# Kernel tuning notes

Measured on AMD Instinct MI355X. Metric: run time of the kernel, lower is better.

The kernel has to match this reference:

```python
import jax, jax.numpy as jnp
import numpy as np
from jax import lax

N = 8192      # nodes == batch (forward cats node and batch embeddings)
E = 262144    # edges, avg degree 32
T = 32        # seq_len
DD = 16       # dynamic_feature_dim
DS = 128      # static_feature_dim
GH = 64       # gnn_hidden_dim
RH = 128      # rnn_hidden_dim
L = 10        # output_lead_times
EPS = 1e-5


def setup_inputs() -> dict:
    key = jax.random.key(0)
    ks = jax.random.split(key, 32)
    def rn(i, shape, s=0.05):
        return jax.random.normal(ks[i], shape, jnp.float32) * s
    return {
        "dynamic_features": rn(0, (N, T, DD), 1.0),
        "x_static": rn(1, (N, DS), 1.0),
        "edge_index": jax.random.randint(ks[2], (2, E), 0, N, jnp.int32),
        "gcn1_w": rn(3, (DS, GH)), "gcn1_b": rn(4, (GH,)),
        "gcn2_w": rn(5, (GH, GH)), "gcn2_b": rn(6, (GH,)),
        "bn1_g": 1.0 + rn(7, (GH,)), "bn1_b": rn(8, (GH,)),
        "bn2_g": 1.0 + rn(9, (GH,)), "bn2_b": rn(10, (GH,)),
        "w_ih0": rn(11, (4 * RH, DD)), "w_hh0": rn(12, (4 * RH, RH)),
        "b_ih0": rn(13, (4 * RH,)), "b_hh0": rn(14, (4 * RH,)),
        "w_ih1": rn(15, (4 * RH, RH)), "w_hh1": rn(16, (4 * RH, RH)),
        "b_ih1": rn(17, (4 * RH,)), "b_hh1": rn(18, (4 * RH,)),
        "fc1_w": rn(19, (GH + RH, 128)), "fc1_b": rn(20, (128,)),
        "fbn_g": 1.0 + rn(21, (128,)), "fbn_b": rn(22, (128,)),
        "fc2_w": rn(23, (128, 64)), "fc2_b": rn(24, (64,)),
        "out_w": rn(25, (64, L)), "out_b": rn(26, (L,)),
    }


def _gcn(x, w, b, src, dst, n):
    h = x @ w
    loops = jnp.arange(n, dtype=src.dtype)
    s = jnp.concatenate([src, loops])
    d = jnp.concatenate([dst, loops])
    deg = jax.ops.segment_sum(jnp.ones(s.shape[0], x.dtype), d, num_segments=n)
    dis = lax.rsqrt(jnp.maximum(deg, 1.0))
    msg = h[s] * (dis[s] * dis[d])[:, None]
    return jax.ops.segment_sum(msg, d, num_segments=n) + b


def _bn(x, g, b):
    # eval-mode BatchNorm1d: running_mean=0, running_var=1
    return x * (g * lax.rsqrt(jnp.asarray(1.0 + EPS, x.dtype))) + b


def _lstm_layer(xp, w_hh):
    # xp: [B, T, 4H] input projection with both biases already added
    B = xp.shape[0]
    H = w_hh.shape[1]
    h0 = jnp.zeros((B, H), xp.dtype)
    c0 = jnp.zeros((B, H), xp.dtype)
    def step(carry, xt):
        h, c = carry
        gates = xt + h @ w_hh.T  # torch gate order: i, f, g, o
        i, f, g, o = jnp.split(gates, 4, axis=-1)
        c = jax.nn.sigmoid(f) * c + jax.nn.sigmoid(i) * jnp.tanh(g)
        h = jax.nn.sigmoid(o) * jnp.tanh(c)
        return (h, c), h
    _, hs = lax.scan(step, (h0, c0), jnp.swapaxes(xp, 0, 1))
    return jnp.swapaxes(hs, 0, 1)  # [B, T, H]


def _forward(dynamic_features, x_static, edge_index,
             gcn1_w, gcn1_b, gcn2_w, gcn2_b, bn1_g, bn1_b, bn2_g, bn2_b,
             w_ih0, w_hh0, b_ih0, b_hh0, w_ih1, w_hh1, b_ih1, b_hh1,
             fc1_w, fc1_b, fbn_g, fbn_b, fc2_w, fc2_b, out_w, out_b):
    src, dst = edge_index[0], edge_index[1]
    n = x_static.shape[0]
    # GNN branch (dropout = eval-mode identity)
    h = _gcn(x_static, gcn1_w, gcn1_b, src, dst, n)
    h = jax.nn.relu(_bn(h, bn1_g, bn1_b))
    h = _gcn(h, gcn2_w, gcn2_b, src, dst, n)
    gnn_emb = jax.nn.relu(_bn(h, bn2_g, bn2_b))
    # 2-layer LSTM branch
    xp0 = jnp.einsum('btd,gd->btg', dynamic_features, w_ih0) + b_ih0 + b_hh0
    h1 = _lstm_layer(xp0, w_hh0)
    xp1 = jnp.einsum('bth,gh->btg', h1, w_ih1) + b_ih1 + b_hh1
    h2 = _lstm_layer(xp1, w_hh1)
    rnn_emb = h2[:, -1, :]
    # fusion MLP
    fused = jnp.concatenate([gnn_emb, rnn_emb], axis=1)
    x = jax.nn.relu(_bn(fused @ fc1_w + fc1_b, fbn_g, fbn_b))
    x = jax.nn.relu(x @ fc2_w + fc2_b)
    return x @ out_w + out_b


def reference(dynamic_features, x_static, edge_index,
              gcn1_w, gcn1_b, gcn2_w, gcn2_b, bn1_g, bn1_b, bn2_g, bn2_b,
              w_ih0, w_hh0, b_ih0, b_hh0, w_ih1, w_hh1, b_ih1, b_hh1,
              fc1_w, fc1_b, fbn_g, fbn_b, fc2_w, fc2_b, out_w, out_b):
    return _forward(dynamic_features, x_static, edge_index,
                    gcn1_w, gcn1_b, gcn2_w, gcn2_b, bn1_g, bn1_b, bn2_g, bn2_b,
                    w_ih0, w_hh0, b_ih0, b_hh0, w_ih1, w_hh1, b_ih1, b_hh1,
                    fc1_w, fc1_b, fbn_g, fbn_b, fc2_w, fc2_b, out_w, out_b)
```

## Files before the change

### kernel.cpp

```cpp
#include <hip/hip_runtime.h>
#include <hip/hip_bf16.h>

#define NN 8192
#define NE 262144

typedef float v2 __attribute__((ext_vector_type(2)));
typedef float v4 __attribute__((ext_vector_type(4)));
typedef float f4 __attribute__((ext_vector_type(4)));
typedef _Float16 h8 __attribute__((ext_vector_type(8)));
typedef _Float16 h4 __attribute__((ext_vector_type(4)));

__device__ __forceinline__ float rcp_(float x) { return __builtin_amdgcn_rcpf(x); }
__device__ __forceinline__ float ew(float iv, float fv, float gv, float ov, float& c) {
    float F = __expf(-fv);
    float I = __expf(-iv);
    float G = __expf(2.0f * gv);
    c = c * rcp_(1.0f + F) + (G - 1.0f) * rcp_((G + 1.0f) * (1.0f + I));
    float O = __expf(-ov);
    float E = __expf(2.0f * c);
    return (E - 1.0f) * rcp_((E + 1.0f) * (1.0f + O));
}

__global__ void k_prep_all(const float* __restrict__ dyn,
                           const float* __restrict__ wih0, const float* __restrict__ whh0,
                           const float* __restrict__ bih0, const float* __restrict__ bhh0,
                           const float* __restrict__ wih1, const float* __restrict__ whh1,
                           const float* __restrict__ bih1, const float* __restrict__ bhh1,
                           const int* __restrict__ dst,
                           _Float16* __restrict__ dyn16, _Float16* __restrict__ WB0h,
                           _Float16* __restrict__ TLg, _Float16* __restrict__ WB1,
                           float* __restrict__ bias, int* __restrict__ cnt) {
    int b = blockIdx.x, tid = threadIdx.x;
    if (b < 4096) {
        int i = b * 256 + tid;
        f4 v = *(const f4*)(dyn + (size_t)i * 4);
        h4 o = {(_Float16)v[0], (_Float16)v[1], (_Float16)v[2], (_Float16)v[3]};
        *(h4*)(dyn16 + (size_t)i * 4) = o;
    } else if (b < 4900) {
        int i = (b - 4096) * 256 + tid;
        if (i < 65536) {
            int idx = i & 7, col = (i >> 3) & 511, kgq = (i >> 12) & 3, kt = i >> 14;
            int kh = kt * 32 + kgq * 8 + idx;
            WB0h[i] = (_Float16)whh0[col * 128 + kh];
        } else if (i < 73728) {
            int m = i - 65536;
            int kd = m & 15, g = m >> 4;
            TLg[m] = (_Float16)wih0[g * 16 + kd];
        } else if (i < 204800) {
            int m = i - 73728;
            int kt = m >> 14, rem = m & 16383, g = rem >> 5, kk = rem & 31, k = kt * 32 + kk;
            WB1[m] = (_Float16)((k < 128) ? wih1[g * 128 + k] : whh1[g * 128 + (k - 128)]);
        } else {
            int g = i - 204800;
            bias[g] = (g < 512) ? (bih0[g] + bhh0[g]) : (bih1[g - 512] + bhh1[g - 512]);
        }
    } else {
        int e = (b - 4900) * 256 + tid;
        if (e < NE) atomicAdd(&cnt[dst[e]], 1);
    }
}

__global__ __launch_bounds__(1024) void k_scan(const int* __restrict__ cnt, int* __restrict__ rowstart,
                                               float* __restrict__ dis) {
    __shared__ int part[1024];
    int t = threadIdx.x;
    int base = t * 8, s = 0, loc[8];
#pragma unroll
    for (int i = 0; i < 8; ++i) { loc[i] = s; s += cnt[base + i]; }
    part[t] = s;
    __syncthreads();
    for (int off = 1; off < 1024; off <<= 1) {
        int v = part[t];
        int add = (t >= off) ? part[t - off] : 0;
        __syncthreads();
        part[t] = v + add;
        __syncthreads();
    }
    int pre = (t == 0) ? 0 : part[t - 1];
#pragma unroll
    for (int i = 0; i < 8; ++i) {
        rowstart[base + i] = pre + loc[i];
        dis[base + i] = rsqrtf((float)(cnt[base + i] + 1));
    }
    if (t == 1023) rowstart[8192] = NE;
}
__global__ void k_fill(const int* __restrict__ src, const int* __restrict__ dst,
                       const int* __restrict__ rowstart, int* __restrict__ cursor,
                       int* __restrict__ srcidx) {
    int e = blockIdx.x * 256 + threadIdx.x;
    if (e < NE) {
        int d = dst[e];
        int pos = rowstart[d] + atomicAdd(&cursor[d], 1);
        srcidx[pos] = src[e];
    }
}
__global__ __launch_bounds__(256) void k_gcn_gemm(const float* __restrict__ in, const float* __restrict__ w,
                                                  const float* __restrict__ dis, float* __restrict__ hs, int K) {
    int wv = threadIdx.x >> 6, ln = threadIdx.x & 63;
    int row = blockIdx.x * 4 + wv;
    const float* xp = in + (size_t)row * K;
    float a = 0.f;
#pragma unroll 4
    for (int k = 0; k < K; ++k) a += xp[k] * w[k * 64 + ln];
    hs[(size_t)row * 64 + ln] = a * dis[row];
}
__global__ __launch_bounds__(256) void k_gather_gemm(const float* __restrict__ hs, const int* __restrict__ srcidx,
                                                     const int* __restrict__ rowstart, const float* __restrict__ dis,
                                                     const float* __restrict__ gb, const float* __restrict__ bng,
                                                     const float* __restrict__ bnb, const float* __restrict__ g2w,
                                                     float* __restrict__ hs2) {
    int ln = threadIdx.x & 63;
    int d = (blockIdx.x * 256 + threadIdx.x) >> 6;
    float acc = hs[(size_t)d * 64 + ln];
    int b = rowstart[d], e = rowstart[d + 1];
    int i = b;
    for (; i + 4 <= e; i += 4) {
        int s0 = srcidx[i], s1 = srcidx[i + 1], s2 = srcidx[i + 2], s3 = srcidx[i + 3];
        acc += hs[(size_t)s0 * 64 + ln];
        acc += hs[(size_t)s1 * 64 + ln];
        acc += hs[(size_t)s2 * 64 + ln];
        acc += hs[(size_t)s3 * 64 + ln];
    }
    for (; i < e; ++i) acc += hs[(size_t)srcidx[i] * 64 + ln];
    float rs = rsqrtf(1.0f + 1e-5f);
    float y = acc * dis[d] + gb[ln];
    y = fmaxf(y * (bng[ln] * rs) + bnb[ln], 0.f);
    float a2 = 0.f;
#pragma unroll 8
    for (int k = 0; k < 64; ++k) a2 += __shfl(y, k, 64) * g2w[k * 64 + ln];
    hs2[(size_t)d * 64 + ln] = a2 * dis[d];
}
__global__ __launch_bounds__(256) void k_gather(const float* __restrict__ hs, const int* __restrict__ srcidx,
                                                const int* __restrict__ rowstart, const float* __restrict__ dis,
                                                const float* __restrict__ gb, const float* __restrict__ bng,
                                                const float* __restrict__ bnb, float* __restrict__ out) {
    int ln = threadIdx.x & 63;
    int d = (blockIdx.x * 256 + threadIdx.x) >> 6;
    float acc = hs[(size_t)d * 64 + ln];
    int b = rowstart[d], e = rowstart[d + 1];
    int i = b;
    for (; i + 4 <= e; i += 4) {
        int s0 = srcidx[i], s1 = srcidx[i + 1], s2 = srcidx[i + 2], s3 = srcidx[i + 3];
        acc += hs[(size_t)s0 * 64 + ln];
        acc += hs[(size_t)s1 * 64 + ln];
        acc += hs[(size_t)s2 * 64 + ln];
        acc += hs[(size_t)s3 * 64 + ln];
    }
    for (; i < e; ++i) acc += hs[(size_t)srcidx[i] * 64 + ln];
    float rs = rsqrtf(1.0f + 1e-5f);
    float v = acc * dis[d] + gb[ln];
    v = v * (bng[ln] * rs) + bnb[ln];
    out[(size_t)d * 64 + ln] = fmaxf(v, 0.f);
}

__device__ __forceinline__ h8 ldx(const _Float16* xs, int buf, int row, int chunk) {
    return *(const h8*)((const char*)xs + buf * 16384 + row * 512 + ((chunk ^ (row & 7)) << 4));
}
__device__ __forceinline__ void wrx(_Float16* xs, int buf, int row, int col, _Float16 v) {
    *(_Float16*)((char*)xs + buf * 16384 + row * 512 + ((((col >> 3) ^ (row & 7))) << 4) + (col & 7) * 2) = v;
}

__global__ __launch_bounds__(512, 2) void k_lstm(const _Float16* __restrict__ dyn16,
                                                 const _Float16* __restrict__ WB0h,
                                                 const _Float16* __restrict__ TLg,
                                                 const _Float16* __restrict__ WB1,
                                                 const float* __restrict__ bias,
                                                 float* __restrict__ rnn) {
    __shared__ __align__(16) _Float16 wb0[65536];
    __shared__ __align__(16) _Float16 xs[16384];

    const int tid = threadIdx.x;
    const int wv = tid >> 6, ln = tid & 63;
    const int lr = ln & 15, kg = ln >> 4;
    const int j = wv * 16 + lr;
    const int row0 = blockIdx.x * 32;

    for (int i = tid; i < 8192; i += 512) ((v4*)wb0)[i] = ((const v4*)WB0h)[i];
    for (int i = tid; i < 16384; i += 512) xs[i] = (_Float16)0.f;

    h8 b1r[8][4];
#pragma unroll
    for (int kt = 0; kt < 8; ++kt)
#pragma unroll
        for (int q = 0; q < 4; ++q)
            b1r[kt][q] = *(const h8*)(WB1 + (size_t)kt * 16384 + (q * 128 + j) * 32 + kg * 8);
    h8 bt[4];
#pragma unroll
    for (int q = 0; q < 4; ++q)
        bt[q] = *(const h8*)(TLg + (q * 128 + j) * 16 + (kg & 1) * 8);

    float b0q[4], b1q[4];
#pragma unroll
    for (int q = 0; q < 4; ++q) { b0q[q] = bias[q * 128 + j]; b1q[q] = bias[512 + q * 128 + j]; }
    float c0[2][4], c1[2][4];
#pragma unroll
    for (int mt = 0; mt < 2; ++mt)
#pragma unroll
        for (int r = 0; r < 4; ++r) { c0[mt][r] = 0.f; c1[mt][r] = 0.f; }

    h8 dreg[2];
#pragma unroll
    for (int mt = 0; mt < 2; ++mt)
#pragma unroll
        for (int e = 0; e < 8; ++e) dreg[mt][e] = (_Float16)0.f;
    if (kg < 2) {
#pragma unroll
        for (int mt = 0; mt < 2; ++mt)
            dreg[mt] = *(const h8*)(dyn16 + (size_t)(row0 + mt * 16 + lr) * 512 + (kg & 1) * 8);
    }
    __syncthreads();

    {
        f4 acc[2][4];
#pragma unroll
        for (int q = 0; q < 4; ++q) { f4 z = {b0q[q], b0q[q], b0q[q], b0q[q]}; acc[0][q] = z; acc[1][q] = z; }
#pragma unroll
        for (int q = 0; q < 4; ++q) {
            acc[0][q] = __builtin_amdgcn_mfma_f32_16x16x32_f16(dreg[0], bt[q], acc[0][q], 0, 0, 0);
            acc[1][q] = __builtin_amdgcn_mfma_f32_16x16x32_f16(dreg[1], bt[q], acc[1][q], 0, 0, 0);
        }
#pragma unroll
        for (int mt = 0; mt < 2; ++mt)
#pragma unroll
            for (int r = 0; r < 4; ++r) {
                float h = ew(acc[mt][0][r], acc[mt][1][r], acc[mt][2][r], acc[mt][3][r], c0[mt][r]);
                wrx(xs, 0, mt * 16 + kg * 4 + r, j, (_Float16)h);
            }
        if (kg < 2) {
#pragma unroll
            for (int mt = 0; mt < 2; ++mt)
                dreg[mt] = *(const h8*)(dyn16 + (size_t)(row0 + mt * 16 + lr) * 512 + 16 + (kg & 1) * 8);
        }
    }

#pragma unroll 1
    for (int i = 0; i < 31; ++i) {
        const int cur = i & 1, old = cur ^ 1;
        __syncthreads();
        f4 acc[2][4];
#pragma unroll
        for (int q = 0; q < 4; ++q) { f4 z = {b1q[q], b1q[q], b1q[q], b1q[q]}; acc[0][q] = z; acc[1][q] = z; }
#pragma unroll
        for (int kt = 0; kt < 8; ++kt) {
            const int bufA = (kt < 4) ? cur : old;
            const int ch = (kt < 4) ? (kt * 4 + kg) : (16 + (kt - 4) * 4 + kg);
            h8 a0 = ldx(xs, bufA, lr, ch);
            h8 a1 = ldx(xs, bufA, 16 + lr, ch);
#pragma unroll
            for (int q = 0; q < 4; ++q) {
                acc[0][q] = __builtin_amdgcn_mfma_f32_16x16x32_f16(a0, b1r[kt][q], acc[0][q], 0, 0, 0);
                acc[1][q] = __builtin_amdgcn_mfma_f32_16x16x32_f16(a1, b1r[kt][q], acc[1][q], 0, 0, 0);
            }
        }
#pragma unroll
        for (int mt = 0; mt < 2; ++mt)
#pragma unroll
            for (int r = 0; r < 4; ++r) {
                float h = ew(acc[mt][0][r], acc[mt][1][r], acc[mt][2][r], acc[mt][3][r], c1[mt][r]);
                wrx(xs, cur, mt * 16 + kg * 4 + r, 128 + j, (_Float16)h);
            }
#pragma unroll
        for (int q = 0; q < 4; ++q) { f4 z = {b0q[q], b0q[q], b0q[q], b0q[q]}; acc[0][q] = z; acc[1][q] = z; }
#pragma unroll
        for (int kt = 0; kt < 4; ++kt) {
            h8 a0 = ldx(xs, cur, lr, kt * 4 + kg);
            h8 a1 = ldx(xs, cur, 16 + lr, kt * 4 + kg);
            h8 bq[4];
#pragma unroll
            for (int q = 0; q < 4; ++q)
                bq[q] = *(const h8*)(wb0 + (size_t)(((kt * 4 + kg) * 512 + q * 128 + j) * 8));
#pragma unroll
            for (int q = 0; q < 4; ++q) {
                acc[0][q] = __builtin_amdgcn_mfma_f32_16x16x32_f16(a0, bq[q], acc[0][q], 0, 0, 0);
                acc[1][q] = __builtin_amdgcn_mfma_f32_16x16x32_f16(a1, bq[q], acc[1][q], 0, 0, 0);
            }
        }
#pragma unroll
        for (int q = 0; q < 4; ++q) {
            acc[0][q] = __builtin_amdgcn_mfma_f32_16x16x32_f16(dreg[0], bt[q], acc[0][q], 0, 0, 0);
            acc[1][q] = __builtin_amdgcn_mfma_f32_16x16x32_f16(dreg[1], bt[q], acc[1][q], 0, 0, 0);
        }
#pragma unroll
        for (int mt = 0; mt < 2; ++mt)
#pragma unroll
            for (int r = 0; r < 4; ++r) {
                float h = ew(acc[mt][0][r], acc[mt][1][r], acc[mt][2][r], acc[mt][3][r], c0[mt][r]);
                wrx(xs, old, mt * 16 + kg * 4 + r, j, (_Float16)h);
            }
        if (i < 30 && kg < 2) {
#pragma unroll
            for (int mt = 0; mt < 2; ++mt)
                dreg[mt] = *(const h8*)(dyn16 + (size_t)(row0 + mt * 16 + lr) * 512 + (i + 2) * 16 + (kg & 1) * 8);
        }
    }
    __syncthreads();
    {
        const int cur = 1, old = 0;
        f4 acc[2][4];
#pragma unroll
        for (int q = 0; q < 4; ++q) { f4 z = {b1q[q], b1q[q], b1q[q], b1q[q]}; acc[0][q] = z; acc[1][q] = z; }
#pragma unroll
        for (int kt = 0; kt < 8; ++kt) {
            const int bufA = (kt < 4) ? cur : old;
            const int ch = (kt < 4) ? (kt * 4 + kg) : (16 + (kt - 4) * 4 + kg);
            h8 a0 = ldx(xs, bufA, lr, ch);
            h8 a1 = ldx(xs, bufA, 16 + lr, ch);
#pragma unroll
            for (int q = 0; q < 4; ++q) {
                acc[0][q] = __builtin_amdgcn_mfma_f32_16x16x32_f16(a0, b1r[kt][q], acc[0][q], 0, 0, 0);
                acc[1][q] = __builtin_amdgcn_mfma_f32_16x16x32_f16(a1, b1r[kt][q], acc[1][q], 0, 0, 0);
            }
        }
#pragma unroll
        for (int mt = 0; mt < 2; ++mt)
#pragma unroll
            for (int r = 0; r < 4; ++r) {
                float h = ew(acc[mt][0][r], acc[mt][1][r], acc[mt][2][r], acc[mt][3][r], c1[mt][r]);
                rnn[(size_t)(row0 + mt * 16 + kg * 4 + r) * 128 + j] = h;
            }
    }
}

__global__ __launch_bounds__(256) void k_head(const float* __restrict__ gnn, const float* __restrict__ rnn,
                                              const float* __restrict__ fc1w, const float* __restrict__ fc1b,
                                              const float* __restrict__ fbng, const float* __restrict__ fbnb,
                                              const float* __restrict__ fc2w, const float* __restrict__ fc2b,
                                              const float* __restrict__ outw, const float* __restrict__ outb,
                                              float* __restrict__ out) {
    __shared__ __align__(16) float xin[32][196];
    __shared__ __align__(16) float xh2[32][132];
    __shared__ __align__(16) float xh3[32][68];
    const int tid = threadIdx.x;
    const int r0 = blockIdx.x * 32;
    for (int i = tid; i < 32 * 64; i += 256) { int r = i >> 6, c = i & 63; xin[r][c] = gnn[(size_t)(r0 + r) * 64 + c]; }
    for (int i = tid; i < 32 * 128; i += 256) { int r = i >> 7, c = i & 127; xin[r][64 + c] = rnn[(size_t)(r0 + r) * 128 + c]; }
    __syncthreads();
    const int wv = tid >> 6, ln = tid & 63, wr = wv * 8;
    const float rs = rsqrtf(1.0f + 1e-5f);
    float a[8][2];
    float b0 = fc1b[2 * ln], b1 = fc1b[2 * ln + 1];
#pragma unroll
    for (int r = 0; r < 8; ++r) { a[r][0] = b0; a[r][1] = b1; }
    for (int k = 0; k < 192; ++k) {
        v2 w = *(const v2*)&fc1w[k * 128 + 2 * ln];
#pragma unroll
        for (int r = 0; r < 8; ++r) { float x = xin[wr + r][k]; a[r][0] += x * w[0]; a[r][1] += x * w[1]; }
    }
    float s0 = fbng[2 * ln] * rs, s1 = fbng[2 * ln + 1] * rs;
    float bb0 = fbnb[2 * ln], bb1 = fbnb[2 * ln + 1];
#pragma unroll
    for (int r = 0; r < 8; ++r) {
        v2 h;
        h[0] = fmaxf(a[r][0] * s0 + bb0, 0.f);
        h[1] = fmaxf(a[r][1] * s1 + bb1, 0.f);
        *(v2*)&xh2[wr + r][2 * ln] = h;
    }
    __syncthreads();
    float a2[8];
    float b2 = fc2b[ln];
#pragma unroll
    for (int r = 0; r < 8; ++r) a2[r] = b2;
    for (int k = 0; k < 128; ++k) {
        float w = fc2w[k * 64 + ln];
#pragma unroll
        for (int r = 0; r < 8; ++r) a2[r] += xh2[wr + r][k] * w;
    }
#pragma unroll
    for (int r = 0; r < 8; ++r) xh3[wr + r][ln] = fmaxf(a2[r], 0.f);
    __syncthreads();
    if (ln < 10) {
#pragma unroll
        for (int r = 0; r < 8; ++r) {
            float a3 = outb[ln];
            for (int k = 0; k < 64; ++k) a3 += xh3[wr + r][k] * outw[k * 10 + ln];
            out[(size_t)(r0 + wr + r) * 10 + ln] = a3;
        }
    }
}

extern "C" void kernel_launch(void* const* d_in, const int* in_sizes, int n_in,
                              void* d_out, int out_size, void* d_ws, size_t ws_size,
                              hipStream_t stream) {
    const float* dyn  = (const float*)d_in[0];
    const float* xs_  = (const float*)d_in[1];
    const int*   ei   = (const int*)d_in[2];
    const float* g1w  = (const float*)d_in[3];
    const float* g1b  = (const float*)d_in[4];
    const float* g2w  = (const float*)d_in[5];
    const float* g2b  = (const float*)d_in[6];
    const float* bn1g = (const float*)d_in[7];
    const float* bn1b = (const float*)d_in[8];
    const float* bn2g = (const float*)d_in[9];
    const float* bn2b = (const float*)d_in[10];
    const float* wih0 = (const float*)d_in[11];
    const float* whh0 = (const float*)d_in[12];
    const float* bih0 = (const float*)d_in[13];
    const float* bhh0 = (const float*)d_in[14];
    const float* wih1 = (const float*)d_in[15];
    const float* whh1 = (const float*)d_in[16];
    const float* bih1 = (const float*)d_in[17];
    const float* bhh1 = (const float*)d_in[18];
    const float* fc1w = (const float*)d_in[19];
    const float* fc1b = (const float*)d_in[20];
    const float* fbng = (const float*)d_in[21];
    const float* fbnb = (const float*)d_in[22];
    const float* fc2w = (const float*)d_in[23];
    const float* fc2b = (const float*)d_in[24];
    const float* outw = (const float*)d_in[25];
    const float* outb = (const float*)d_in[26];
    float* out = (float*)d_out;

    char* ws = (char*)d_ws;
    _Float16* WB0h  = (_Float16*)(ws + 0);
    _Float16* TLg   = (_Float16*)(ws + 131072);
    _Float16* WB1   = (_Float16*)(ws + 147456);
    _Float16* dyn16 = (_Float16*)(ws + 409600);
    float* fbase = (float*)(ws + 8798208);
    float* bias = fbase;
    float* dis  = fbase + 1024;
    float* hs   = fbase + 9216;
    float* hs2  = fbase + 533504;
    float* gnn  = fbase + 1057792;
    float* rnn  = fbase + 1582080;
    int* ibase   = (int*)(ws + 19320832);
    int* cnt     = ibase;
    int* cursor  = ibase + 8192;
    int* rowstart= ibase + 16384;
    int* srcidx  = ibase + 24592;

    const int* srcp = ei;
    const int* dstp = ei + NE;

    hipMemsetAsync(cnt, 0, 2 * 8192 * sizeof(int), stream);
    k_prep_all<<<5924, 256, 0, stream>>>(dyn, wih0, whh0, bih0, bhh0, wih1, whh1, bih1, bhh1,
                                         dstp, dyn16, WB0h, TLg, WB1, bias, cnt);
    k_scan<<<1, 1024, 0, stream>>>(cnt, rowstart, dis);
    k_fill<<<1024, 256, 0, stream>>>(srcp, dstp, rowstart, cursor, srcidx);
    k_gcn_gemm<<<2048, 256, 0, stream>>>(xs_, g1w, dis, hs, 128);
    k_gather_gemm<<<2048, 256, 0, stream>>>(hs, srcidx, rowstart, dis, g1b, bn1g, bn1b, g2w, hs2);
    k_gather<<<2048, 256, 0, stream>>>(hs2, srcidx, rowstart, dis, g2b, bn2g, bn2b, gnn);
    k_lstm<<<256, 512, 0, stream>>>(dyn16, WB0h, TLg, WB1, bias, rnn);
    k_head<<<256, 256, 0, stream>>>(gnn, rnn, fc1w, fc1b, fbng, fbnb, fc2w, fc2b, outw, outb, out);
}
```

Baseline: 297.4 us.

## Fold first GCN GEMM into prep kernel, rework LSTM activations and prefetch

The first GCN projection now runs inside the prep kernel as extra blocks, without degree scaling. This removes one kernel launch and lets the GEMM overlap with the edge counting. Because of that, the gather kernels now multiply each neighbour row by dis[s], which adds a per-edge load. The LSTM cell math is rewritten with separate sigmoid and tanh helpers, and the dynamic-feature prefetch for step i+2 is moved to the start of the loop body to hide its latency. The new activations use more exp and reciprocal calls than the old fused formula.

Result: slower. 311.2 us (+4.6%).

```diff
diff --git a/kernel.cpp b/kernel.cpp
--- a/kernel.cpp
+++ b/kernel.cpp
@@ -11,15 +11,8 @@
 typedef _Float16 h4 __attribute__((ext_vector_type(4)));
 
 __device__ __forceinline__ float rcp_(float x) { return __builtin_amdgcn_rcpf(x); }
-__device__ __forceinline__ float ew(float iv, float fv, float gv, float ov, float& c) {
-    float F = __expf(-fv);
-    float I = __expf(-iv);
-    float G = __expf(2.0f * gv);
-    c = c * rcp_(1.0f + F) + (G - 1.0f) * rcp_((G + 1.0f) * (1.0f + I));
-    float O = __expf(-ov);
-    float E = __expf(2.0f * c);
-    return (E - 1.0f) * rcp_((E + 1.0f) * (1.0f + O));
-}
+__device__ __forceinline__ float sigm(float x) { return rcp_(1.0f + __expf(-x)); }
+__device__ __forceinline__ float tanh_(float x) { return 1.0f - 2.0f * rcp_(__expf(2.0f * x) + 1.0f); }
 
 __global__ void k_prep_all(const float* __restrict__ dyn,
                            const float* __restrict__ wih0, const float* __restrict__ whh0,
@@ -27,9 +20,11 @@
                            const float* __restrict__ wih1, const float* __restrict__ whh1,
                            const float* __restrict__ bih1, const float* __restrict__ bhh1,
                            const int* __restrict__ dst,
+                           const float* __restrict__ xs_, const float* __restrict__ g1w,
                            _Float16* __restrict__ dyn16, _Float16* __restrict__ WB0h,
                            _Float16* __restrict__ TLg, _Float16* __restrict__ WB1,
-                           float* __restrict__ bias, int* __restrict__ cnt) {
+                           float* __restrict__ bias, int* __restrict__ cnt,
+                           float* __restrict__ hs_raw) {
     int b = blockIdx.x, tid = threadIdx.x;
     if (b < 4096) {
         int i = b * 256 + tid;
@@ -54,9 +49,17 @@
             int g = i - 204800;
             bias[g] = (g < 512) ? (bih0[g] + bhh0[g]) : (bih1[g - 512] + bhh1[g - 512]);
         }
-    } else {
+    } else if (b < 5924) {
         int e = (b - 4900) * 256 + tid;
         if (e < NE) atomicAdd(&cnt[dst[e]], 1);
+    } else {
+        int wv = tid >> 6, ln = tid & 63;
+        int row = (b - 5924) * 4 + wv;
+        const float* xp = xs_ + (size_t)row * 128;
+        float a = 0.f;
+#pragma unroll 4
+        for (int k = 0; k < 128; ++k) a += xp[k] * g1w[k * 64 + ln];
+        hs_raw[(size_t)row * 64 + ln] = a;
     }
 }
 
@@ -94,16 +97,6 @@
         srcidx[pos] = src[e];
     }
 }
-__global__ __launch_bounds__(256) void k_gcn_gemm(const float* __restrict__ in, const float* __restrict__ w,
-                                                  const float* __restrict__ dis, float* __restrict__ hs, int K) {
-    int wv = threadIdx.x >> 6, ln = threadIdx.x & 63;
-    int row = blockIdx.x * 4 + wv;
-    const float* xp = in + (size_t)row * K;
-    float a = 0.f;
-#pragma unroll 4
-    for (int k = 0; k < K; ++k) a += xp[k] * w[k * 64 + ln];
-    hs[(size_t)row * 64 + ln] = a * dis[row];
-}
 __global__ __launch_bounds__(256) void k_gather_gemm(const float* __restrict__ hs, const int* __restrict__ srcidx,
                                                      const int* __restrict__ rowstart, const float* __restrict__ dis,
                                                      const float* __restrict__ gb, const float* __restrict__ bng,
@@ -111,24 +104,25 @@
                                                      float* __restrict__ hs2) {
     int ln = threadIdx.x & 63;
     int d = (blockIdx.x * 256 + threadIdx.x) >> 6;
-    float acc = hs[(size_t)d * 64 + ln];
+    float dd = dis[d];
+    float acc = hs[(size_t)d * 64 + ln] * dd;
     int b = rowstart[d], e = rowstart[d + 1];
     int i = b;
     for (; i + 4 <= e; i += 4) {
         int s0 = srcidx[i], s1 = srcidx[i + 1], s2 = srcidx[i + 2], s3 = srcidx[i + 3];
-        acc += hs[(size_t)s0 * 64 + ln];
-        acc += hs[(size_t)s1 * 64 + ln];
-        acc += hs[(size_t)s2 * 64 + ln];
-        acc += hs[(size_t)s3 * 64 + ln];
-    }
-    for (; i < e; ++i) acc += hs[(size_t)srcidx[i] * 64 + ln];
+        acc += hs[(size_t)s0 * 64 + ln] * dis[s0];
+        acc += hs[(size_t)s1 * 64 + ln] * dis[s1];
+        acc += hs[(size_t)s2 * 64 + ln] * dis[s2];
+        acc += hs[(size_t)s3 * 64 + ln] * dis[s3];
+    }
+    for (; i < e; ++i) { int s = srcidx[i]; acc += hs[(size_t)s * 64 + ln] * dis[s]; }
     float rs = rsqrtf(1.0f + 1e-5f);
-    float y = acc * dis[d] + gb[ln];
+    float y = acc * dd + gb[ln];
     y = fmaxf(y * (bng[ln] * rs) + bnb[ln], 0.f);
     float a2 = 0.f;
 #pragma unroll 8
     for (int k = 0; k < 64; ++k) a2 += __shfl(y, k, 64) * g2w[k * 64 + ln];
-    hs2[(size_t)d * 64 + ln] = a2 * dis[d];
+    hs2[(size_t)d * 64 + ln] = a2;
 }
 __global__ __launch_bounds__(256) void k_gather(const float* __restrict__ hs, const int* __restrict__ srcidx,
                                                 const int* __restrict__ rowstart, const float* __restrict__ dis,
@@ -136,19 +130,20 @@
                                                 const float* __restrict__ bnb, float* __restrict__ out) {
     int ln = threadIdx.x & 63;
     int d = (blockIdx.x * 256 + threadIdx.x) >> 6;
-    float acc = hs[(size_t)d * 64 + ln];
+    float dd = dis[d];
+    float acc = hs[(size_t)d * 64 + ln] * dd;
     int b = rowstart[d], e = rowstart[d + 1];
     int i = b;
     for (; i + 4 <= e; i += 4) {
         int s0 = srcidx[i], s1 = srcidx[i + 1], s2 = srcidx[i + 2], s3 = srcidx[i + 3];
-        acc += hs[(size_t)s0 * 64 + ln];
-        acc += hs[(size_t)s1 * 64 + ln];
-        acc += hs[(size_t)s2 * 64 + ln];
-        acc += hs[(size_t)s3 * 64 + ln];
-    }
-    for (; i < e; ++i) acc += hs[(size_t)srcidx[i] * 64 + ln];
+        acc += hs[(size_t)s0 * 64 + ln] * dis[s0];
+        acc += hs[(size_t)s1 * 64 + ln] * dis[s1];
+        acc += hs[(size_t)s2 * 64 + ln] * dis[s2];
+        acc += hs[(size_t)s3 * 64 + ln] * dis[s3];
+    }
+    for (; i < e; ++i) { int s = srcidx[i]; acc += hs[(size_t)s * 64 + ln] * dis[s]; }
     float rs = rsqrtf(1.0f + 1e-5f);
-    float v = acc * dis[d] + gb[ln];
+    float v = acc * dd + gb[ln];
     v = v * (bng[ln] * rs) + bnb[ln];
     out[(size_t)d * 64 + ln] = fmaxf(v, 0.f);
 }
@@ -198,11 +193,11 @@
 #pragma unroll
         for (int r = 0; r < 4; ++r) { c0[mt][r] = 0.f; c1[mt][r] = 0.f; }
 
-    h8 dreg[2];
+    h8 dreg[2], pre[2];
 #pragma unroll
     for (int mt = 0; mt < 2; ++mt)
 #pragma unroll
-        for (int e = 0; e < 8; ++e) dreg[mt][e] = (_Float16)0.f;
+        for (int e = 0; e < 8; ++e) { dreg[mt][e] = (_Float16)0.f; pre[mt][e] = (_Float16)0.f; }
     if (kg < 2) {
 #pragma unroll
         for (int mt = 0; mt < 2; ++mt)
@@ -223,8 +218,10 @@
         for (int mt = 0; mt < 2; ++mt)
 #pragma unroll
             for (int r = 0; r < 4; ++r) {
-                float h = ew(acc[mt][0][r], acc[mt][1][r], acc[mt][2][r], acc[mt][3][r], c0[mt][r]);
-                wrx(xs, 0, mt * 16 + kg * 4 + r, j, (_Float16)h);
+                float iv = acc[mt][0][r], fv = acc[mt][1][r], gv = acc[mt][2][r], ov = acc[mt][3][r];
+                float c = sigm(fv) * c0[mt][r] + sigm(iv) * tanh_(gv);
+                c0[mt][r] = c;
+                wrx(xs, 0, mt * 16 + kg * 4 + r, j, (_Float16)(sigm(ov) * tanh_(c)));
             }
         if (kg < 2) {
 #pragma unroll
@@ -237,6 +234,11 @@
     for (int i = 0; i < 31; ++i) {
         const int cur = i & 1, old = cur ^ 1;
         __syncthreads();
+        if (i < 30 && kg < 2) {
+#pragma unroll
+            for (int mt = 0; mt < 2; ++mt)
+                pre[mt] = *(const h8*)(dyn16 + (size_t)(row0 + mt * 16 + lr) * 512 + (i + 2) * 16 + (kg & 1) * 8);
+        }
         f4 acc[2][4];
 #pragma unroll
         for (int q = 0; q < 4; ++q) { f4 z = {b1q[q], b1q[q], b1q[q], b1q[q]}; acc[0][q] = z; acc[1][q] = z; }
@@ -256,8 +258,10 @@
         for (int mt = 0; mt < 2; ++mt)
 #pragma unroll
             for (int r = 0; r < 4; ++r) {
-                float h = ew(acc[mt][0][r], acc[mt][1][r], acc[mt][2][r], acc[mt][3][r], c1[mt][r]);
-                wrx(xs, cur, mt * 16 + kg * 4 + r, 128 + j, (_Float16)h);
+                float iv = acc[mt][0][r], fv = acc[mt][1][r], gv = acc[mt][2][r], ov = acc[mt][3][r];
+                float c = sigm(fv) * c1[mt][r] + sigm(iv) * tanh_(gv);
+                c1[mt][r] = c;
+                wrx(xs, cur, mt * 16 + kg * 4 + r, 128 + j, (_Float16)(sigm(ov) * tanh_(c)));
             }
 #pragma unroll
         for (int q = 0; q < 4; ++q) { f4 z = {b0q[q], b0q[q], b0q[q], b0q[q]}; acc[0][q] = z; acc[1][q] = z; }
@@ -284,14 +288,12 @@
         for (int mt = 0; mt < 2; ++mt)
 #pragma unroll
             for (int r = 0; r < 4; ++r) {
-                float h = ew(acc[mt][0][r], acc[mt][1][r], acc[mt][2][r], acc[mt][3][r], c0[mt][r]);
-                wrx(xs, old, mt * 16 + kg * 4 + r, j, (_Float16)h);
-            }
-        if (i < 30 && kg < 2) {
-#pragma unroll
-            for (int mt = 0; mt < 2; ++mt)
-                dreg[mt] = *(const h8*)(dyn16 + (size_t)(row0 + mt * 16 + lr) * 512 + (i + 2) * 16 + (kg & 1) * 8);
-        }
+                float iv = acc[mt][0][r], fv = acc[mt][1][r], gv = acc[mt][2][r], ov = acc[mt][3][r];
+                float c = sigm(fv) * c0[mt][r] + sigm(iv) * tanh_(gv);
+                c0[mt][r] = c;
+                wrx(xs, old, mt * 16 + kg * 4 + r, j, (_Float16)(sigm(ov) * tanh_(c)));
+            }
+        if (i < 30) { dreg[0] = pre[0]; dreg[1] = pre[1]; }
     }
     __syncthreads();
     {
@@ -315,7 +317,9 @@
         for (int mt = 0; mt < 2; ++mt)
 #pragma unroll
             for (int r = 0; r < 4; ++r) {
-                float h = ew(acc[mt][0][r], acc[mt][1][r], acc[mt][2][r], acc[mt][3][r], c1[mt][r]);
+                float iv = acc[mt][0][r], fv = acc[mt][1][r], gv = acc[mt][2][r], ov = acc[mt][3][r];
+                float c = sigm(fv) * c1[mt][r] + sigm(iv) * tanh_(gv);
+                float h = sigm(ov) * tanh_(c);
                 rnn[(size_t)(row0 + mt * 16 + kg * 4 + r) * 128 + j] = h;
             }
     }
@@ -432,11 +436,10 @@
     const int* dstp = ei + NE;
 
     hipMemsetAsync(cnt, 0, 2 * 8192 * sizeof(int), stream);
-    k_prep_all<<<5924, 256, 0, stream>>>(dyn, wih0, whh0, bih0, bhh0, wih1, whh1, bih1, bhh1,
-                                         dstp, dyn16, WB0h, TLg, WB1, bias, cnt);
+    k_prep_all<<<7972, 256, 0, stream>>>(dyn, wih0, whh0, bih0, bhh0, wih1, whh1, bih1, bhh1,
+                                         dstp, xs_, g1w, dyn16, WB0h, TLg, WB1, bias, cnt, hs);
     k_scan<<<1, 1024, 0, stream>>>(cnt, rowstart, dis);
     k_fill<<<1024, 256, 0, stream>>>(srcp, dstp, rowstart, cursor, srcidx);
-    k_gcn_gemm<<<2048, 256, 0, stream>>>(xs_, g1w, dis, hs, 128);
     k_gather_gemm<<<2048, 256, 0, stream>>>(hs, srcidx, rowstart, dis, g1b, bn1g, bn1b, g2w, hs2);
     k_gather<<<2048, 256, 0, stream>>>(hs2, srcidx, rowstart, dis, g2b, bn2g, bn2b, gnn);
     k_lstm<<<256, 512, 0, stream>>>(dyn16, WB0h, TLg, WB1, bias, rnn);
```
